# Optimization experiments

Measured on AMD Instinct MI355X. Metric: run time of the kernel, lower is better.

## Reference

```python
import jax, jax.numpy as jnp
import numpy as np

EPS = 1e-6
CONV_P = 3.0
GM_P = 2.0
NUM_NODES = 50000
NUM_EDGES = 600000
NUM_GRAPHS = 512
IN_DIM = 128
HID = 128
OUT_DIM = 64


def _scatter_mean(vals, index, num_segments):
    # scatter_mean with empty segments -> 0 (count clamped to 1)
    s = jax.ops.segment_sum(vals, index, num_segments=num_segments)
    cnt = jax.ops.segment_sum(jnp.ones((vals.shape[0],), vals.dtype), index,
                              num_segments=num_segments)
    return s / jnp.maximum(cnt, 1.0)[:, None]


def _signed_pow(v, p):
    return jnp.sign(v) * (jnp.abs(v) + EPS) ** p


def _spm_conv(x, W, b, src, dst, p):
    h = x @ W.T + b                      # [N, hid] linear
    msg = h[src]                          # gather x_j  [E, hid]
    t = _signed_pow(msg, p)
    pooled = _scatter_mean(t, dst, NUM_NODES)
    return _signed_pow(pooled, 1.0 / p)


def setup_inputs() -> dict:
    key = jax.random.key(0)
    ks = jax.random.split(key, 8)
    x = jax.random.normal(ks[0], (NUM_NODES, IN_DIM), jnp.float32)
    edge_index = jax.random.randint(ks[1], (2, NUM_EDGES), 0, NUM_NODES)
    batch = jnp.sort(jax.random.randint(ks[2], (NUM_NODES,), 0, NUM_GRAPHS))
    s1 = 1.0 / np.sqrt(IN_DIM)
    s2 = 1.0 / np.sqrt(HID)
    W1 = jax.random.uniform(ks[3], (HID, IN_DIM), jnp.float32, -s1, s1)
    b1 = jax.random.uniform(ks[4], (HID,), jnp.float32, -s1, s1)
    W2 = jax.random.uniform(ks[5], (HID, HID), jnp.float32, -s2, s2)
    b2 = jax.random.uniform(ks[6], (HID,), jnp.float32, -s2, s2)
    # final layer: orthogonal-init frozen weight (out_dim=64, hid=128)
    A = jax.random.normal(ks[7], (HID, OUT_DIM), jnp.float32)
    Q, _ = jnp.linalg.qr(A)
    Wout = Q.T                            # [OUT_DIM, HID], orthonormal rows
    bout = jax.random.uniform(jax.random.fold_in(key, 9), (OUT_DIM,),
                              jnp.float32, -s2, s2)
    return {"x": x, "W1": W1, "b1": b1, "W2": W2, "b2": b2,
            "Wout": Wout, "bout": bout, "edge_index": edge_index,
            "batch": batch}


def reference(x, W1, b1, W2, b2, Wout, bout, edge_index, batch):
    src, dst = edge_index[0], edge_index[1]
    h = _spm_conv(x, W1, b1, src, dst, CONV_P)
    h = jax.nn.relu(h)                    # relu between conv layers only
    h = _spm_conv(h, W2, b2, src, dst, CONV_P)
    # global generalized mean pool (signed)
    t = _signed_pow(h, GM_P)
    pooled = _scatter_mean(t, batch, NUM_GRAPHS)
    graph_repr = _signed_pow(pooled, 1.0 / GM_P)   # [G, HID]
    return graph_repr @ Wout.T + bout              # [G, OUT_DIM]
```

## Files before the change

kernel.cpp:

```cpp
#include <hip/hip_runtime.h>
#include <hip/hip_bf16.h>
#include <math.h>

#define N_NODES 50000
#define N_EDGES 600000
#define N_GRAPHS 512
#define DIM 128
#define OUTD 64
#define EPSV 1e-6f
#define BSTRIDE 64
#define EBLK 2344
#define LIN_BLK 782

typedef __attribute__((ext_vector_type(8))) short bf16x8;
typedef __attribute__((ext_vector_type(4))) float f32x4;

__device__ __forceinline__ float sgn(float v) {
    return (v > 0.f) ? 1.f : ((v < 0.f) ? -1.f : 0.f);
}

__device__ __forceinline__ float cube_signed(float v) {
    float m = fabsf(v) + EPSV;
    return sgn(v) * m * m * m;
}

__device__ __forceinline__ float cbrt_pos(float m) {
    return exp2f(log2f(m) * (1.0f / 3.0f));
}

__device__ __forceinline__ unsigned short f2bf(float f) {
    unsigned u = __float_as_uint(f);
    unsigned r = (u + 0x7fff + ((u >> 16) & 1)) >> 16;
    return (unsigned short)r;
}

__device__ __forceinline__ float bf2f(unsigned short h) {
    return __uint_as_float(((unsigned)h) << 16);
}

__device__ __forceinline__ void gather_acc8(const unsigned* __restrict__ T32,
                                            const int* __restrict__ bucket,
                                            int cnt16, int lane, float2 acc[4]) {
    #pragma unroll
    for (int j = 0; j < 4; j++) acc[j] = make_float2(0.f, 0.f);
    if (cnt16 <= 0) return;
    int myidx = bucket[lane];
    int sub = lane & 15, grp = lane >> 4;
    for (int i = 0; i < cnt16; i += 16) {
        uint4 u[4];
        #pragma unroll
        for (int c = 0; c < 4; c++) {
            int s = __shfl(myidx, i + c * 4 + grp, 64);
            u[c] = *(const uint4*)(T32 + (size_t)s * 64 + sub * 4);
        }
        #pragma unroll
        for (int c = 0; c < 4; c++) {
            acc[0].x += __uint_as_float(u[c].x << 16);
            acc[0].y += __uint_as_float(u[c].x & 0xffff0000u);
            acc[1].x += __uint_as_float(u[c].y << 16);
            acc[1].y += __uint_as_float(u[c].y & 0xffff0000u);
            acc[2].x += __uint_as_float(u[c].z << 16);
            acc[2].y += __uint_as_float(u[c].z & 0xffff0000u);
            acc[3].x += __uint_as_float(u[c].w << 16);
            acc[3].y += __uint_as_float(u[c].w & 0xffff0000u);
        }
    }
    #pragma unroll
    for (int j = 0; j < 4; j++) {
        acc[j].x += __shfl_xor(acc[j].x, 16, 64);
        acc[j].y += __shfl_xor(acc[j].y, 16, 64);
        acc[j].x += __shfl_xor(acc[j].x, 32, 64);
        acc[j].y += __shfl_xor(acc[j].y, 32, 64);
    }
}

__device__ __forceinline__ float acc_pick_x(const float2 acc[4], int grp) {
    return grp == 0 ? acc[0].x : grp == 1 ? acc[1].x : grp == 2 ? acc[2].x : acc[3].x;
}
__device__ __forceinline__ float acc_pick_y(const float2 acc[4], int grp) {
    return grp == 0 ? acc[0].y : grp == 1 ? acc[1].y : grp == 2 ? acc[2].y : acc[3].y;
}


__global__ void prep(const float* __restrict__ W1, const float* __restrict__ W2,
                     unsigned short* __restrict__ W1hi, unsigned short* __restrict__ W1lo,
                     unsigned short* __restrict__ W2hi, unsigned short* __restrict__ W2lo,
                     int* __restrict__ deg,
                     const int* __restrict__ batch, int* __restrict__ gstart,
                     unsigned* __restrict__ T1z, unsigned* __restrict__ T2z) {
    int i = blockIdx.x * 256 + threadIdx.x;
    {
        float w = W1[i];
        unsigned short h = f2bf(w);
        W1hi[i] = h;
        W1lo[i] = f2bf(w - bf2f(h));
        w = W2[i];
        h = f2bf(w);
        W2hi[i] = h;
        W2lo[i] = f2bf(w - bf2f(h));
    }
    if (i < 64) { T1z[i] = 0u; T2z[i] = 0u; }
    if (i <= N_GRAPHS) {
        int lo = 0, hi = N_NODES;
        while (lo < hi) {
            int mid = (lo + hi) >> 1;
            if (batch[mid] < i) lo = mid + 1; else hi = mid;
        }
        gstart[i] = lo;
    }
    for (int j = i; j < N_NODES; j += 16384) deg[j] = 0;
}


__global__ __launch_bounds__(256) void edges_lin1(const int* __restrict__ src,
                                                  const int* __restrict__ dst,
                                                  int* __restrict__ deg,
                                                  int* __restrict__ csr,
                                                  const float* __restrict__ X,
                                                  const unsigned short* __restrict__ Whi,
                                                  const unsigned short* __restrict__ Wlo,
                                                  const float* __restrict__ B,
                                                  unsigned short* __restrict__ T) {
    int b = blockIdx.x;
    if (b < EBLK) {
        int e = b * 256 + threadIdx.x;
        if (e < N_EDGES) {
            int d = dst[e];
            int slot = atomicAdd(&deg[d], 1);
            if (slot < BSTRIDE) csr[d * BSTRIDE + slot] = src[e] + 1;
        }
        return;
    }
    int wave = threadIdx.x >> 6;
    int lane = threadIdx.x & 63;
    int tile = (b - EBLK) * 4 + wave;
    if (tile >= N_NODES / 16) return;
    int n0 = tile * 16;
    int r = lane & 15;
    int g = lane >> 4;

    bf16x8 xh[4], xl[4];
    const float* xrow = X + (size_t)(n0 + r) * DIM + g * 8;
    #pragma unroll
    for (int kb = 0; kb < 4; kb++) {
        float4 a = *(const float4*)(xrow + kb * 32);
        float4 bb = *(const float4*)(xrow + kb * 32 + 4);
        float v[8] = {a.x, a.y, a.z, a.w, bb.x, bb.y, bb.z, bb.w};
        #pragma unroll
        for (int j = 0; j < 8; j++) {
            unsigned short h = f2bf(v[j]);
            float rem = v[j] - bf2f(h);
            xh[kb][j] = (short)h;
            xl[kb][j] = (short)f2bf(rem);
        }
    }

    #pragma unroll
    for (int ct = 0; ct < 8; ct++) {
        const unsigned short* whbase = Whi + (size_t)(ct * 16 + r) * DIM + g * 8;
        const unsigned short* wlbase = Wlo + (size_t)(ct * 16 + r) * DIM + g * 8;
        f32x4 acc = {0.f, 0.f, 0.f, 0.f};
        #pragma unroll
        for (int kb = 0; kb < 4; kb++) {
            bf16x8 wh = *(const bf16x8*)(whbase + kb * 32);
            bf16x8 wl = *(const bf16x8*)(wlbase + kb * 32);
            acc = __builtin_amdgcn_mfma_f32_16x16x32_bf16(xh[kb], wh, acc, 0, 0, 0);
            acc = __builtin_amdgcn_mfma_f32_16x16x32_bf16(xl[kb], wh, acc, 0, 0, 0);
            acc = __builtin_amdgcn_mfma_f32_16x16x32_bf16(xh[kb], wl, acc, 0, 0, 0);
        }
        float bias = B[ct * 16 + r];
        #pragma unroll
        for (int q = 0; q < 4; q++) {
            int node = g * 4 + q;
            float h = acc[q] + bias;
            T[(size_t)(n0 + node + 1) * DIM + ct * 16 + r] = f2bf(cube_signed(h));
        }
    }
}


__global__ __launch_bounds__(512) void agg_linear_cube(const unsigned* __restrict__ T32,
                                                       const int* __restrict__ deg,
                                                       const int* __restrict__ csr,
                                                       const unsigned short* __restrict__ Whi,
                                                       const unsigned short* __restrict__ Wlo,
                                                       const float* __restrict__ B,
                                                       unsigned short* __restrict__ Tout) {
    __shared__ __attribute__((aligned(16))) unsigned Phi[16][68];
    __shared__ __attribute__((aligned(16))) unsigned Plo[16][68];
    int wave = threadIdx.x >> 6;
    int lane = threadIdx.x & 63;
    int n0 = blockIdx.x * 16;
    int sub = lane & 15, grp = lane >> 4;

    #pragma unroll
    for (int q = 0; q < 2; q++) {
        int row = wave * 2 + q;
        int nd = n0 + row;
        int d = deg[nd];
        int cnt = d < BSTRIDE ? d : BSTRIDE;
        int cnt16 = (cnt + 15) & ~15;
        float2 acc[4];
        gather_acc8(T32, csr + (size_t)nd * BSTRIDE, cnt16, lane, acc);
        float c = (float)(d > 1 ? d : 1);
        float m0 = acc_pick_x(acc, grp) / c;
        float m1 = acc_pick_y(acc, grp) / c;
        float r0 = fmaxf(sgn(m0) * cbrt_pos(fabsf(m0) + EPSV), 0.f);
        float r1 = fmaxf(sgn(m1) * cbrt_pos(fabsf(m1) + EPSV), 0.f);
        unsigned short h0 = f2bf(r0), h1 = f2bf(r1);
        unsigned short l0 = f2bf(r0 - bf2f(h0)), l1 = f2bf(r1 - bf2f(h1));
        Phi[row][sub * 4 + grp] = (unsigned)h0 | ((unsigned)h1 << 16);
        Plo[row][sub * 4 + grp] = (unsigned)l0 | ((unsigned)l1 << 16);
    }
    __syncthreads();

    int r = lane & 15;
    int g = lane >> 4;
    bf16x8 xh[4], xl[4];
    #pragma unroll
    for (int kb = 0; kb < 4; kb++) {
        xh[kb] = *(const bf16x8*)&Phi[r][kb * 16 + g * 4];
        xl[kb] = *(const bf16x8*)&Plo[r][kb * 16 + g * 4];
    }
    int ct = wave;
    const unsigned short* whbase = Whi + (size_t)(ct * 16 + r) * DIM + g * 8;
    const unsigned short* wlbase = Wlo + (size_t)(ct * 16 + r) * DIM + g * 8;
    f32x4 acc = {0.f, 0.f, 0.f, 0.f};
    #pragma unroll
    for (int kb = 0; kb < 4; kb++) {
        bf16x8 wh = *(const bf16x8*)(whbase + kb * 32);
        bf16x8 wl = *(const bf16x8*)(wlbase + kb * 32);
        acc = __builtin_amdgcn_mfma_f32_16x16x32_bf16(xh[kb], wh, acc, 0, 0, 0);
        acc = __builtin_amdgcn_mfma_f32_16x16x32_bf16(xl[kb], wh, acc, 0, 0, 0);
        acc = __builtin_amdgcn_mfma_f32_16x16x32_bf16(xh[kb], wl, acc, 0, 0, 0);
    }
    float bias = B[ct * 16 + r];
    #pragma unroll
    for (int q = 0; q < 4; q++) {
        int node = g * 4 + q;
        float h = acc[q] + bias;
        Tout[(size_t)(n0 + node + 1) * DIM + ct * 16 + r] = f2bf(cube_signed(h));
    }
}


__global__ __launch_bounds__(256) void aggregate(const unsigned* __restrict__ T32,
                                                 const int* __restrict__ deg,
                                                 const int* __restrict__ csr,
                                                 float* __restrict__ P) {
    int nd = blockIdx.x * 4 + (threadIdx.x >> 6);
    if (nd >= N_NODES) return;
    int lane = threadIdx.x & 63;
    int sub = lane & 15, grp = lane >> 4;
    int d = deg[nd];
    int cnt = d < BSTRIDE ? d : BSTRIDE;
    int cnt16 = (cnt + 15) & ~15;
    float2 acc[4];
    gather_acc8(T32, csr + (size_t)nd * BSTRIDE, cnt16, lane, acc);
    float c = (float)(d > 1 ? d : 1);
    float m0 = acc_pick_x(acc, grp) / c;
    float m1 = acc_pick_y(acc, grp) / c;
    float r0 = sgn(m0) * cbrt_pos(fabsf(m0) + EPSV);
    float r1 = sgn(m1) * cbrt_pos(fabsf(m1) + EPSV);
    *(float2*)(P + (size_t)nd * DIM + sub * 8 + grp * 2) = make_float2(r0, r1);
}


__global__ __launch_bounds__(128) void pool_final(const float* __restrict__ P,
                                                  const int* __restrict__ gstart,
                                                  const float* __restrict__ Wout,
                                                  const float* __restrict__ bout,
                                                  float* __restrict__ out) {
    __shared__ float R[DIM];
    __shared__ float partial[128];
    int g = blockIdx.x, f = threadIdx.x;
    int s = gstart[g], e = gstart[g + 1];
    float acc = 0.f;
    for (int i = s; i < e; i++) {
        float v = P[(size_t)i * DIM + f];
        float m = fabsf(v) + EPSV;
        acc += sgn(v) * m * m;
    }
    int cnt = e - s;
    float c = (float)(cnt > 1 ? cnt : 1);
    float mean = acc / c;
    R[f] = sgn(mean) * sqrtf(fabsf(mean) + EPSV);
    __syncthreads();

    int o = f & 63;
    int half = f >> 6;
    const float4* W4 = (const float4*)Wout + o * 32 + half * 16;
    const float4* R4 = (const float4*)R + half * 16;
    float a = 0.f;
    #pragma unroll
    for (int k = 0; k < 16; k++) {
        float4 w = W4[k];
        float4 r = R4[k];
        a += r.x * w.x + r.y * w.y + r.z * w.z + r.w * w.w;
    }
    partial[f] = a;
    __syncthreads();
    if (f < OUTD) out[(size_t)g * OUTD + f] = bout[f] + partial[f] + partial[f + 64];
}


extern "C" void kernel_launch(void* const* d_in, const int* in_sizes, int n_in,
                              void* d_out, int out_size, void* d_ws, size_t ws_size,
                              hipStream_t stream) {
    const float* x    = (const float*)d_in[0];
    const float* W1   = (const float*)d_in[1];
    const float* b1   = (const float*)d_in[2];
    const float* W2   = (const float*)d_in[3];
    const float* b2   = (const float*)d_in[4];
    const float* Wout = (const float*)d_in[5];
    const float* bout = (const float*)d_in[6];
    const int* edge   = (const int*)d_in[7];
    const int* batch  = (const int*)d_in[8];
    const int* srcp = edge;
    const int* dstp = edge + N_EDGES;
    float* out = (float*)d_out;

    char* ws = (char*)d_ws;
    size_t off = 0;
    auto alloc = [&](size_t bytes) -> char* {
        char* p = ws + off;
        off += (bytes + 255) / 256 * 256;
        return p;
    };
    unsigned short* T1 = (unsigned short*)alloc((size_t)(N_NODES + 1) * DIM * 2);
    unsigned short* T2 = (unsigned short*)alloc((size_t)(N_NODES + 1) * DIM * 2);
    float* P        = (float*)alloc((size_t)N_NODES * DIM * 4);
    int*   deg      = (int*)alloc((size_t)N_NODES * 4);
    int*   csr      = (int*)alloc((size_t)N_NODES * BSTRIDE * 4);
    int*   gstart   = (int*)alloc((size_t)(N_GRAPHS + 1) * 4);
    unsigned short* W1hi = (unsigned short*)alloc((size_t)DIM * DIM * 2);
    unsigned short* W1lo = (unsigned short*)alloc((size_t)DIM * DIM * 2);
    unsigned short* W2hi = (unsigned short*)alloc((size_t)DIM * DIM * 2);
    unsigned short* W2lo = (unsigned short*)alloc((size_t)DIM * DIM * 2);

    hipMemsetAsync(csr, 0, (size_t)N_NODES * BSTRIDE * 4, stream);
    prep<<<64, 256, 0, stream>>>(W1, W2, W1hi, W1lo, W2hi, W2lo,
                                 deg, batch, gstart,
                                 (unsigned*)T1, (unsigned*)T2);
    edges_lin1<<<EBLK + LIN_BLK, 256, 0, stream>>>(srcp, dstp, deg, csr,
                                                   x, W1hi, W1lo, b1, T1);

    const int TILES = N_NODES / 16;
    const int ABLK = (N_NODES + 3) / 4;
    agg_linear_cube<<<TILES, 512, 0, stream>>>((const unsigned*)T1, deg, csr,
                                               W2hi, W2lo, b2, T2);
    aggregate<<<ABLK, 256, 0, stream>>>((const unsigned*)T2, deg, csr, P);
    pool_final<<<N_GRAPHS, 128, 0, stream>>>(P, gstart, Wout, bout, out);
}
```

Baseline: 189.5 us.

## Store CSR buckets as uint16, drop the CSR memset, split edge build from linear

The per-node neighbour buckets now hold 16-bit source indices instead of 32-bit ints, which halves the CSR footprint and its traffic. The 12.8 MB hipMemsetAsync that zeroed the CSR is removed. Instead, the gather masks lanes beyond the node's degree and points them at the zero row 0 of the feature table. The fused edge-build plus first-linear kernel is split into two separate launches. That split adds a launch and gives up any overlap the fused kernel allowed between the atomic CSR build and the MFMA linear.

```diff
diff --git a/kernel.cpp b/kernel.cpp
--- a/kernel.cpp
+++ b/kernel.cpp
@@ -10,7 +10,6 @@
 #define EPSV 1e-6f
 #define BSTRIDE 64
 #define EBLK 2344
-#define LIN_BLK 782
 
 typedef __attribute__((ext_vector_type(8))) short bf16x8;
 typedef __attribute__((ext_vector_type(4))) float f32x4;
@@ -39,13 +38,14 @@
 }
 
 __device__ __forceinline__ void gather_acc8(const unsigned* __restrict__ T32,
-                                            const int* __restrict__ bucket,
-                                            int cnt16, int lane, float2 acc[4]) {
+                                            const unsigned short* __restrict__ bucket,
+                                            int cnt, int lane, float2 acc[4]) {
     #pragma unroll
     for (int j = 0; j < 4; j++) acc[j] = make_float2(0.f, 0.f);
-    if (cnt16 <= 0) return;
-    int myidx = bucket[lane];
+    if (cnt <= 0) return;
+    int myidx = (lane < cnt) ? (int)bucket[lane] : 0;
     int sub = lane & 15, grp = lane >> 4;
+    int cnt16 = (cnt + 15) & ~15;
     for (int i = 0; i < cnt16; i += 16) {
         uint4 u[4];
         #pragma unroll
@@ -112,28 +112,25 @@
 }
 
 
-__global__ __launch_bounds__(256) void edges_lin1(const int* __restrict__ src,
-                                                  const int* __restrict__ dst,
-                                                  int* __restrict__ deg,
-                                                  int* __restrict__ csr,
-                                                  const float* __restrict__ X,
-                                                  const unsigned short* __restrict__ Whi,
-                                                  const unsigned short* __restrict__ Wlo,
-                                                  const float* __restrict__ B,
-                                                  unsigned short* __restrict__ T) {
-    int b = blockIdx.x;
-    if (b < EBLK) {
-        int e = b * 256 + threadIdx.x;
-        if (e < N_EDGES) {
-            int d = dst[e];
-            int slot = atomicAdd(&deg[d], 1);
-            if (slot < BSTRIDE) csr[d * BSTRIDE + slot] = src[e] + 1;
-        }
-        return;
-    }
+__global__ void build(const int* __restrict__ src, const int* __restrict__ dst,
+                      int* __restrict__ deg, unsigned short* __restrict__ csr) {
+    int e = blockIdx.x * 256 + threadIdx.x;
+    if (e < N_EDGES) {
+        int d = dst[e];
+        int slot = atomicAdd(&deg[d], 1);
+        if (slot < BSTRIDE) csr[d * BSTRIDE + slot] = (unsigned short)(src[e] + 1);
+    }
+}
+
+
+__global__ __launch_bounds__(256) void linear_cube_mfma(const float* __restrict__ X,
+                                                        const unsigned short* __restrict__ Whi,
+                                                        const unsigned short* __restrict__ Wlo,
+                                                        const float* __restrict__ B,
+                                                        unsigned short* __restrict__ T) {
     int wave = threadIdx.x >> 6;
     int lane = threadIdx.x & 63;
-    int tile = (b - EBLK) * 4 + wave;
+    int tile = blockIdx.x * 4 + wave;
     if (tile >= N_NODES / 16) return;
     int n0 = tile * 16;
     int r = lane & 15;
@@ -144,8 +141,8 @@
     #pragma unroll
     for (int kb = 0; kb < 4; kb++) {
         float4 a = *(const float4*)(xrow + kb * 32);
-        float4 bb = *(const float4*)(xrow + kb * 32 + 4);
-        float v[8] = {a.x, a.y, a.z, a.w, bb.x, bb.y, bb.z, bb.w};
+        float4 b = *(const float4*)(xrow + kb * 32 + 4);
+        float v[8] = {a.x, a.y, a.z, a.w, b.x, b.y, b.z, b.w};
         #pragma unroll
         for (int j = 0; j < 8; j++) {
             unsigned short h = f2bf(v[j]);
@@ -181,7 +178,7 @@
 
 __global__ __launch_bounds__(512) void agg_linear_cube(const unsigned* __restrict__ T32,
                                                        const int* __restrict__ deg,
-                                                       const int* __restrict__ csr,
+                                                       const unsigned short* __restrict__ csr,
                                                        const unsigned short* __restrict__ Whi,
                                                        const unsigned short* __restrict__ Wlo,
                                                        const float* __restrict__ B,
@@ -199,9 +196,8 @@
         int nd = n0 + row;
         int d = deg[nd];
         int cnt = d < BSTRIDE ? d : BSTRIDE;
-        int cnt16 = (cnt + 15) & ~15;
         float2 acc[4];
-        gather_acc8(T32, csr + (size_t)nd * BSTRIDE, cnt16, lane, acc);
+        gather_acc8(T32, csr + (size_t)nd * BSTRIDE, cnt, lane, acc);
         float c = (float)(d > 1 ? d : 1);
         float m0 = acc_pick_x(acc, grp) / c;
         float m1 = acc_pick_y(acc, grp) / c;
@@ -246,7 +242,7 @@
 
 __global__ __launch_bounds__(256) void aggregate(const unsigned* __restrict__ T32,
                                                  const int* __restrict__ deg,
-                                                 const int* __restrict__ csr,
+                                                 const unsigned short* __restrict__ csr,
                                                  float* __restrict__ P) {
     int nd = blockIdx.x * 4 + (threadIdx.x >> 6);
     if (nd >= N_NODES) return;
@@ -254,9 +250,8 @@
     int sub = lane & 15, grp = lane >> 4;
     int d = deg[nd];
     int cnt = d < BSTRIDE ? d : BSTRIDE;
-    int cnt16 = (cnt + 15) & ~15;
     float2 acc[4];
-    gather_acc8(T32, csr + (size_t)nd * BSTRIDE, cnt16, lane, acc);
+    gather_acc8(T32, csr + (size_t)nd * BSTRIDE, cnt, lane, acc);
     float c = (float)(d > 1 ? d : 1);
     float m0 = acc_pick_x(acc, grp) / c;
     float m1 = acc_pick_y(acc, grp) / c;
@@ -331,22 +326,22 @@
     unsigned short* T2 = (unsigned short*)alloc((size_t)(N_NODES + 1) * DIM * 2);
     float* P        = (float*)alloc((size_t)N_NODES * DIM * 4);
     int*   deg      = (int*)alloc((size_t)N_NODES * 4);
-    int*   csr      = (int*)alloc((size_t)N_NODES * BSTRIDE * 4);
+    unsigned short* csr = (unsigned short*)alloc((size_t)N_NODES * BSTRIDE * 2);
     int*   gstart   = (int*)alloc((size_t)(N_GRAPHS + 1) * 4);
     unsigned short* W1hi = (unsigned short*)alloc((size_t)DIM * DIM * 2);
     unsigned short* W1lo = (unsigned short*)alloc((size_t)DIM * DIM * 2);
     unsigned short* W2hi = (unsigned short*)alloc((size_t)DIM * DIM * 2);
     unsigned short* W2lo = (unsigned short*)alloc((size_t)DIM * DIM * 2);
 
-    hipMemsetAsync(csr, 0, (size_t)N_NODES * BSTRIDE * 4, stream);
     prep<<<64, 256, 0, stream>>>(W1, W2, W1hi, W1lo, W2hi, W2lo,
                                  deg, batch, gstart,
                                  (unsigned*)T1, (unsigned*)T2);
-    edges_lin1<<<EBLK + LIN_BLK, 256, 0, stream>>>(srcp, dstp, deg, csr,
-                                                   x, W1hi, W1lo, b1, T1);
+    build<<<EBLK, 256, 0, stream>>>(srcp, dstp, deg, csr);
 
     const int TILES = N_NODES / 16;
+    const int LBLK = (TILES + 3) / 4;
     const int ABLK = (N_NODES + 3) / 4;
+    linear_cube_mfma<<<LBLK, 256, 0, stream>>>(x, W1hi, W1lo, b1, T1);
     agg_linear_cube<<<TILES, 512, 0, stream>>>((const unsigned*)T1, deg, csr,
                                                W2hi, W2lo, b2, T2);
     aggregate<<<ABLK, 256, 0, stream>>>((const unsigned*)T2, deg, csr, P);
```

Measured after the change: 186.3 us. No clear change (-1.7%).
